# Optimization experiments

Hardware: AMD Instinct MI355X
Metric: run time of the kernel (lower is better)

## Reference

```python
import jax, jax.numpy as jnp
import numpy as np

BLOCK_SIZE = 64
HIDDEN = 1024
INTERMEDIATE = 4096
NUM_BLOCK = HIDDEN // BLOCK_SIZE              # 16
INT_BLOCK = (INTERMEDIATE // HIDDEN) * BLOCK_SIZE  # 256


def setup_inputs() -> dict:
    key = jax.random.key(0)
    k_x, k_w1, k_b1, k_w2, k_b2 = jax.random.split(key, 5)
    hidden_states = jax.random.normal(k_x, (4, 2048, HIDDEN), dtype=jnp.float32)
    w1 = 0.02 * jax.random.normal(k_w1, (NUM_BLOCK, INT_BLOCK, BLOCK_SIZE), dtype=jnp.float32)
    b1 = 0.001 * jax.random.normal(k_b1, (INTERMEDIATE,), dtype=jnp.float32)
    w2 = 0.02 * jax.random.normal(k_w2, (NUM_BLOCK, BLOCK_SIZE, INT_BLOCK), dtype=jnp.float32)
    b2 = 0.001 * jax.random.normal(k_b2, (HIDDEN,), dtype=jnp.float32)
    return {"hidden_states": hidden_states, "w1": w1, "b1": b1, "w2": w2, "b2": b2}


def reference(hidden_states, w1, b1, w2, b2):
    lead = hidden_states.shape[:-1]
    dim = hidden_states.shape[-1]
    nb, ibs, bs = w1.shape  # num_block, intermediate_block_size, block_size
    x = hidden_states.reshape(-1, nb, bs)                 # [B, n, i]
    h = jnp.einsum('bni,noi->bno', x, w1)                 # [B, n, o]
    # channel shuffle: transpose block and feature axes before flattening
    h = jnp.swapaxes(h, -1, -2).reshape(-1, nb * ibs)     # [B, o*n order]
    h = jax.nn.gelu(h + b1, approximate=False)
    h = h.reshape(-1, nb, ibs)                            # regroup after shuffle
    y = jnp.einsum('bni,noi->bno', h, w2).reshape(-1, nb * bs) + b2
    return y.reshape(*lead, dim)
```

## Files before the change

kernel.cpp:

```cpp
#include <hip/hip_runtime.h>
#include <hip/hip_bf16.h>


typedef __attribute__((ext_vector_type(8))) short  short8;
typedef __attribute__((ext_vector_type(4))) short  short4v;
typedef __attribute__((ext_vector_type(4))) float  floatx4;

#define XP 1032

__device__ __forceinline__ short f2bf(float f) {
  union { __hip_bfloat16 h; short s; } u;
  u.h = __float2bfloat16(f);
  return u.s;
}
__device__ __forceinline__ float bf2f(short s) {
  union { float f; unsigned u; } uu;
  uu.u = ((unsigned)(unsigned short)s) << 16;
  return uu.f;
}
__device__ __forceinline__ int pk16(float a, float b) {
  return (int)(unsigned short)f2bf(a) | ((int)(unsigned short)f2bf(b) << 16);
}

__device__ __forceinline__ float gelu_f(float v) {
  float m = v * v;
  float c = fmaf(-0.1029375f, m, -2.3020807f);
  float z = v * c;
  float e = __builtin_amdgcn_exp2f(z);
  return v * __builtin_amdgcn_rcpf(1.0f + e);
}

__global__ void pack_k(const float* __restrict__ w1, const float* __restrict__ w2,
                       const float* __restrict__ b1, short* __restrict__ w1p,
                       short* __restrict__ w2p, short* __restrict__ b1p) {
  const int t = blockIdx.x * blockDim.x + threadIdx.x;
  const int lane = t & 63;
  const int lhi = lane >> 4;
  if (t < 32768) {
    const int ks = (t >> 6) & 1, np = (t >> 7) & 15, n = (t >> 11) & 15;
    const float* src = w1 + ((size_t)(n * 256 + np * 16 + (lane & 15)) * 64 + ks * 32 + lhi * 8);
    short8 f;
#pragma unroll
    for (int e = 0; e < 8; ++e) f[e] = f2bf(src[e]);
    *(short8*)(w1p + (size_t)t * 8) = f;
  } else if (t < 65536) {
    const int t2 = t - 32768;
    const int ot = (t2 >> 6) & 3, s = (t2 >> 8) & 7, np = (t2 >> 11) & 15;
    const int op = ot * 16 + (lane & 15);
    short8 f;
#pragma unroll
    for (int e = 0; e < 8; ++e) {
      const int Kc = 32 * s + 16 * ((e >> 2) & 1) + 4 * lhi + (e & 3);
      const int n = Kc >> 4, ohi = Kc & 15;
      f[e] = f2bf(w2[(size_t)(np * 64 + op) * 256 + ohi * 16 + n]);
    }
    *(short8*)(w2p + (size_t)t2 * 8) = f;
  } else {
    const int t3 = t - 65536;
    const int np = (t3 >> 6) & 15, n = (t3 >> 10) & 15;
    short4v b;
#pragma unroll
    for (int r = 0; r < 4; ++r) b[r] = f2bf(b1[(np * 16 + lhi * 4 + r) * 16 + n]);
    *(short4v*)(b1p + (size_t)((n * 16 + np) * 64 + lane) * 4) = b;
  }
}

__global__ __launch_bounds__(256, 4) void fused_k(
    const float* __restrict__ x, const short* __restrict__ w1p,
    const short* __restrict__ w2p, const short* __restrict__ b1p,
    const float* __restrict__ b2, float* __restrict__ y) {
  __shared__ __align__(16) short xs[16 * XP];

  const int tid = threadIdx.x;
  const int wv = tid >> 6, lane = tid & 63;
  const int l15 = lane & 15, lhi = lane >> 4;
  const int rt  = blockIdx.x >> 2;
  const int np  = (blockIdx.x & 3) * 4 + wv;

#pragma unroll
  for (int p = 0; p < 4; ++p) {
    const int row = wv * 4 + p;
#pragma unroll
    for (int q = 0; q < 4; ++q) {
      const int col = q * 256 + lane * 4;
      floatx4 v = *(const floatx4*)(x + (size_t)(rt * 16 + row) * 1024 + col);
      short4v sv;
#pragma unroll
      for (int e = 0; e < 4; ++e) sv[e] = f2bf(v[e]);
      *(short4v*)(&xs[row * XP + col]) = sv;
    }
  }
  __syncthreads();

  floatx4 c0 = {0.f,0.f,0.f,0.f}, c1 = {0.f,0.f,0.f,0.f};
  floatx4 c2 = {0.f,0.f,0.f,0.f}, c3 = {0.f,0.f,0.f,0.f};

#pragma unroll
  for (int s = 0; s < 8; ++s) {
    int pka0, pka1, pkb0, pkb1;

    {
      const int n = 2 * s;
      short8 xf0 = *(const short8*)(&xs[l15 * XP + n * 64 + lhi * 8]);
      short8 xf1 = *(const short8*)(&xs[l15 * XP + n * 64 + 32 + lhi * 8]);
      short8 wf0 = *(const short8*)(w1p + (size_t)(((n * 16 + np) * 2 + 0) * 64 + lane) * 8);
      short8 wf1 = *(const short8*)(w1p + (size_t)(((n * 16 + np) * 2 + 1) * 64 + lane) * 8);
      short4v bv = *(const short4v*)(b1p + (size_t)((n * 16 + np) * 64 + lane) * 4);
      floatx4 acc = {0.f, 0.f, 0.f, 0.f};
      acc = __builtin_amdgcn_mfma_f32_16x16x32_bf16(wf0, xf0, acc, 0, 0, 0);
      acc = __builtin_amdgcn_mfma_f32_16x16x32_bf16(wf1, xf1, acc, 0, 0, 0);
      const float g0 = gelu_f(acc[0] + bf2f(bv[0]));
      const float g1 = gelu_f(acc[1] + bf2f(bv[1]));
      const float g2 = gelu_f(acc[2] + bf2f(bv[2]));
      const float g3 = gelu_f(acc[3] + bf2f(bv[3]));
      pka0 = pk16(g0, g1);
      pka1 = pk16(g2, g3);
    }
    {
      const int n = 2 * s + 1;
      short8 xf0 = *(const short8*)(&xs[l15 * XP + n * 64 + lhi * 8]);
      short8 xf1 = *(const short8*)(&xs[l15 * XP + n * 64 + 32 + lhi * 8]);
      short8 wf0 = *(const short8*)(w1p + (size_t)(((n * 16 + np) * 2 + 0) * 64 + lane) * 8);
      short8 wf1 = *(const short8*)(w1p + (size_t)(((n * 16 + np) * 2 + 1) * 64 + lane) * 8);
      short4v bv = *(const short4v*)(b1p + (size_t)((n * 16 + np) * 64 + lane) * 4);
      floatx4 acc = {0.f, 0.f, 0.f, 0.f};
      acc = __builtin_amdgcn_mfma_f32_16x16x32_bf16(wf0, xf0, acc, 0, 0, 0);
      acc = __builtin_amdgcn_mfma_f32_16x16x32_bf16(wf1, xf1, acc, 0, 0, 0);
      const float g0 = gelu_f(acc[0] + bf2f(bv[0]));
      const float g1 = gelu_f(acc[1] + bf2f(bv[1]));
      const float g2 = gelu_f(acc[2] + bf2f(bv[2]));
      const float g3 = gelu_f(acc[3] + bf2f(bv[3]));
      pkb0 = pk16(g0, g1);
      pkb1 = pk16(g2, g3);
    }

    union { int i[4]; short8 v; } af;
    af.i[0] = pka0; af.i[1] = pka1; af.i[2] = pkb0; af.i[3] = pkb1;
    const size_t wb = (size_t)((np * 8 + s) * 4) * 64 * 8;
    short8 bf0 = *(const short8*)(w2p + wb + (size_t)(0 * 64 + lane) * 8);
    short8 bf1 = *(const short8*)(w2p + wb + (size_t)(1 * 64 + lane) * 8);
    short8 bf2v = *(const short8*)(w2p + wb + (size_t)(2 * 64 + lane) * 8);
    short8 bf3 = *(const short8*)(w2p + wb + (size_t)(3 * 64 + lane) * 8);
    c0 = __builtin_amdgcn_mfma_f32_16x16x32_bf16(af.v, bf0, c0, 0, 0, 0);
    c1 = __builtin_amdgcn_mfma_f32_16x16x32_bf16(af.v, bf1, c1, 0, 0, 0);
    c2 = __builtin_amdgcn_mfma_f32_16x16x32_bf16(af.v, bf2v, c2, 0, 0, 0);
    c3 = __builtin_amdgcn_mfma_f32_16x16x32_bf16(af.v, bf3, c3, 0, 0, 0);
  }

  floatx4 cc[4] = {c0, c1, c2, c3};
#pragma unroll
  for (int ot = 0; ot < 4; ++ot) {
    const int col = np * 64 + ot * 16 + l15;
    const float bb = b2[col];
    float* py = y + (size_t)(rt * 16 + lhi * 4) * 1024 + col;
#pragma unroll
    for (int r = 0; r < 4; ++r)
      py[(size_t)r * 1024] = cc[ot][r] + bb;
  }
}

extern "C" void kernel_launch(void* const* d_in, const int* in_sizes, int n_in,
                              void* d_out, int out_size, void* d_ws, size_t ws_size,
                              hipStream_t stream) {
  const float* x  = (const float*)d_in[0];
  const float* w1 = (const float*)d_in[1];
  const float* b1 = (const float*)d_in[2];
  const float* w2 = (const float*)d_in[3];
  const float* b2 = (const float*)d_in[4];
  float* y = (float*)d_out;

  short* w1p = (short*)d_ws;
  short* w2p = w1p + 16 * 256 * 64;
  short* b1p = w2p + 16 * 256 * 64;

  pack_k<<<160, 512, 0, stream>>>(w1, w2, b1, w1p, w2p, b1p);
  fused_k<<<2048, 256, 0, stream>>>(x, w1p, w2p, b1p, b2, y);
}
```

Baseline: 47.49 us.

## Software-pipeline weight loads with double-buffered registers and remap block order

Replaces the unrolled loop with an explicit two-stage register double buffer: the loads for step s+1 are issued before the compute of step s, with sched_barriers pinning that order. Occupancy drops from 4 to 3 blocks per SIMD to leave room for the extra registers. Block indexing now walks row tiles fastest instead of output slices. Loads of x and stores of y use nontemporal hints. The intent is to hide global weight-load latency behind the MFMA and GELU work, at the cost of higher register pressure, fewer resident waves and different L2 reuse of x across blocks.

```diff
diff --git a/kernel.cpp b/kernel.cpp
--- a/kernel.cpp
+++ b/kernel.cpp
@@ -65,7 +65,49 @@
   }
 }
 
-__global__ __launch_bounds__(256, 4) void fused_k(
+#define DECLF(F) \
+  short8 F##wf00, F##wf01, F##wf10, F##wf11, F##bf0, F##bf1, F##bf2, F##bf3, \
+         F##xa0, F##xa1, F##xb0, F##xb1; \
+  short4v F##bv0, F##bv1;
+
+#define LOADS(F, s) { \
+  const int n0_ = 2 * (s), n1_ = 2 * (s) + 1; \
+  F##wf00 = *(const short8*)(w1p + (size_t)(((n0_ * 16 + np) * 2 + 0) * 64 + lane) * 8); \
+  F##wf01 = *(const short8*)(w1p + (size_t)(((n0_ * 16 + np) * 2 + 1) * 64 + lane) * 8); \
+  F##wf10 = *(const short8*)(w1p + (size_t)(((n1_ * 16 + np) * 2 + 0) * 64 + lane) * 8); \
+  F##wf11 = *(const short8*)(w1p + (size_t)(((n1_ * 16 + np) * 2 + 1) * 64 + lane) * 8); \
+  F##bv0  = *(const short4v*)(b1p + (size_t)((n0_ * 16 + np) * 64 + lane) * 4); \
+  F##bv1  = *(const short4v*)(b1p + (size_t)((n1_ * 16 + np) * 64 + lane) * 4); \
+  F##bf0  = *(const short8*)(w2p + (size_t)(((np * 8 + (s)) * 4 + 0) * 64 + lane) * 8); \
+  F##bf1  = *(const short8*)(w2p + (size_t)(((np * 8 + (s)) * 4 + 1) * 64 + lane) * 8); \
+  F##bf2  = *(const short8*)(w2p + (size_t)(((np * 8 + (s)) * 4 + 2) * 64 + lane) * 8); \
+  F##bf3  = *(const short8*)(w2p + (size_t)(((np * 8 + (s)) * 4 + 3) * 64 + lane) * 8); \
+  F##xa0  = *(const short8*)(&xs[l15 * XP + n0_ * 64 + lhi * 8]); \
+  F##xa1  = *(const short8*)(&xs[l15 * XP + n0_ * 64 + 32 + lhi * 8]); \
+  F##xb0  = *(const short8*)(&xs[l15 * XP + n1_ * 64 + lhi * 8]); \
+  F##xb1  = *(const short8*)(&xs[l15 * XP + n1_ * 64 + 32 + lhi * 8]); \
+}
+
+#define STEPC(F) { \
+  floatx4 a0_ = {0.f,0.f,0.f,0.f}, a1_ = {0.f,0.f,0.f,0.f}; \
+  a0_ = __builtin_amdgcn_mfma_f32_16x16x32_bf16(F##wf00, F##xa0, a0_, 0, 0, 0); \
+  a0_ = __builtin_amdgcn_mfma_f32_16x16x32_bf16(F##wf01, F##xa1, a0_, 0, 0, 0); \
+  a1_ = __builtin_amdgcn_mfma_f32_16x16x32_bf16(F##wf10, F##xb0, a1_, 0, 0, 0); \
+  a1_ = __builtin_amdgcn_mfma_f32_16x16x32_bf16(F##wf11, F##xb1, a1_, 0, 0, 0); \
+  union { int i[4]; short8 v; } af_; \
+  af_.i[0] = pk16(gelu_f(a0_[0] + bf2f(F##bv0[0])), gelu_f(a0_[1] + bf2f(F##bv0[1]))); \
+  af_.i[1] = pk16(gelu_f(a0_[2] + bf2f(F##bv0[2])), gelu_f(a0_[3] + bf2f(F##bv0[3]))); \
+  af_.i[2] = pk16(gelu_f(a1_[0] + bf2f(F##bv1[0])), gelu_f(a1_[1] + bf2f(F##bv1[1]))); \
+  af_.i[3] = pk16(gelu_f(a1_[2] + bf2f(F##bv1[2])), gelu_f(a1_[3] + bf2f(F##bv1[3]))); \
+  c0 = __builtin_amdgcn_mfma_f32_16x16x32_bf16(af_.v, F##bf0, c0, 0, 0, 0); \
+  c1 = __builtin_amdgcn_mfma_f32_16x16x32_bf16(af_.v, F##bf1, c1, 0, 0, 0); \
+  c2 = __builtin_amdgcn_mfma_f32_16x16x32_bf16(af_.v, F##bf2, c2, 0, 0, 0); \
+  c3 = __builtin_amdgcn_mfma_f32_16x16x32_bf16(af_.v, F##bf3, c3, 0, 0, 0); \
+}
+
+#define SB __builtin_amdgcn_sched_barrier(0);
+
+__global__ __launch_bounds__(256, 3) void fused_k(
     const float* __restrict__ x, const short* __restrict__ w1p,
     const short* __restrict__ w2p, const short* __restrict__ b1p,
     const float* __restrict__ b2, float* __restrict__ y) {
@@ -74,8 +116,8 @@
   const int tid = threadIdx.x;
   const int wv = tid >> 6, lane = tid & 63;
   const int l15 = lane & 15, lhi = lane >> 4;
-  const int rt  = blockIdx.x >> 2;
-  const int np  = (blockIdx.x & 3) * 4 + wv;
+  const int rt  = blockIdx.x & 511;
+  const int np  = (blockIdx.x >> 9) * 4 + wv;
 
 #pragma unroll
   for (int p = 0; p < 4; ++p) {
@@ -83,7 +125,8 @@
 #pragma unroll
     for (int q = 0; q < 4; ++q) {
       const int col = q * 256 + lane * 4;
-      floatx4 v = *(const floatx4*)(x + (size_t)(rt * 16 + row) * 1024 + col);
+      floatx4 v = __builtin_nontemporal_load(
+          (const floatx4*)(x + (size_t)(rt * 16 + row) * 1024 + col));
       short4v sv;
 #pragma unroll
       for (int e = 0; e < 4; ++e) sv[e] = f2bf(v[e]);
@@ -95,57 +138,17 @@
   floatx4 c0 = {0.f,0.f,0.f,0.f}, c1 = {0.f,0.f,0.f,0.f};
   floatx4 c2 = {0.f,0.f,0.f,0.f}, c3 = {0.f,0.f,0.f,0.f};
 
-#pragma unroll
-  for (int s = 0; s < 8; ++s) {
-    int pka0, pka1, pkb0, pkb1;
+  DECLF(A) DECLF(B)
 
-    {
-      const int n = 2 * s;
-      short8 xf0 = *(const short8*)(&xs[l15 * XP + n * 64 + lhi * 8]);
-      short8 xf1 = *(const short8*)(&xs[l15 * XP + n * 64 + 32 + lhi * 8]);
-      short8 wf0 = *(const short8*)(w1p + (size_t)(((n * 16 + np) * 2 + 0) * 64 + lane) * 8);
-      short8 wf1 = *(const short8*)(w1p + (size_t)(((n * 16 + np) * 2 + 1) * 64 + lane) * 8);
-      short4v bv = *(const short4v*)(b1p + (size_t)((n * 16 + np) * 64 + lane) * 4);
-      floatx4 acc = {0.f, 0.f, 0.f, 0.f};
-      acc = __builtin_amdgcn_mfma_f32_16x16x32_bf16(wf0, xf0, acc, 0, 0, 0);
-      acc = __builtin_amdgcn_mfma_f32_16x16x32_bf16(wf1, xf1, acc, 0, 0, 0);
-      const float g0 = gelu_f(acc[0] + bf2f(bv[0]));
-      const float g1 = gelu_f(acc[1] + bf2f(bv[1]));
-      const float g2 = gelu_f(acc[2] + bf2f(bv[2]));
-      const float g3 = gelu_f(acc[3] + bf2f(bv[3]));
-      pka0 = pk16(g0, g1);
-      pka1 = pk16(g2, g3);
-    }
-    {
-      const int n = 2 * s + 1;
-      short8 xf0 = *(const short8*)(&xs[l15 * XP + n * 64 + lhi * 8]);
-      short8 xf1 = *(const short8*)(&xs[l15 * XP + n * 64 + 32 + lhi * 8]);
-      short8 wf0 = *(const short8*)(w1p + (size_t)(((n * 16 + np) * 2 + 0) * 64 + lane) * 8);
-      short8 wf1 = *(const short8*)(w1p + (size_t)(((n * 16 + np) * 2 + 1) * 64 + lane) * 8);
-      short4v bv = *(const short4v*)(b1p + (size_t)((n * 16 + np) * 64 + lane) * 4);
-      floatx4 acc = {0.f, 0.f, 0.f, 0.f};
-      acc = __builtin_amdgcn_mfma_f32_16x16x32_bf16(wf0, xf0, acc, 0, 0, 0);
-      acc = __builtin_amdgcn_mfma_f32_16x16x32_bf16(wf1, xf1, acc, 0, 0, 0);
-      const float g0 = gelu_f(acc[0] + bf2f(bv[0]));
-      const float g1 = gelu_f(acc[1] + bf2f(bv[1]));
-      const float g2 = gelu_f(acc[2] + bf2f(bv[2]));
-      const float g3 = gelu_f(acc[3] + bf2f(bv[3]));
-      pkb0 = pk16(g0, g1);
-      pkb1 = pk16(g2, g3);
-    }
-
-    union { int i[4]; short8 v; } af;
-    af.i[0] = pka0; af.i[1] = pka1; af.i[2] = pkb0; af.i[3] = pkb1;
-    const size_t wb = (size_t)((np * 8 + s) * 4) * 64 * 8;
-    short8 bf0 = *(const short8*)(w2p + wb + (size_t)(0 * 64 + lane) * 8);
-    short8 bf1 = *(const short8*)(w2p + wb + (size_t)(1 * 64 + lane) * 8);
-    short8 bf2v = *(const short8*)(w2p + wb + (size_t)(2 * 64 + lane) * 8);
-    short8 bf3 = *(const short8*)(w2p + wb + (size_t)(3 * 64 + lane) * 8);
-    c0 = __builtin_amdgcn_mfma_f32_16x16x32_bf16(af.v, bf0, c0, 0, 0, 0);
-    c1 = __builtin_amdgcn_mfma_f32_16x16x32_bf16(af.v, bf1, c1, 0, 0, 0);
-    c2 = __builtin_amdgcn_mfma_f32_16x16x32_bf16(af.v, bf2v, c2, 0, 0, 0);
-    c3 = __builtin_amdgcn_mfma_f32_16x16x32_bf16(af.v, bf3, c3, 0, 0, 0);
-  }
+  LOADS(A, 0)
+  LOADS(B, 1) SB STEPC(A)
+  LOADS(A, 2) SB STEPC(B)
+  LOADS(B, 3) SB STEPC(A)
+  LOADS(A, 4) SB STEPC(B)
+  LOADS(B, 5) SB STEPC(A)
+  LOADS(A, 6) SB STEPC(B)
+  LOADS(B, 7) SB STEPC(A)
+  SB STEPC(B)
 
   floatx4 cc[4] = {c0, c1, c2, c3};
 #pragma unroll
@@ -155,7 +158,7 @@
     float* py = y + (size_t)(rt * 16 + lhi * 4) * 1024 + col;
 #pragma unroll
     for (int r = 0; r < 4; ++r)
-      py[(size_t)r * 1024] = cc[ot][r] + bb;
+      __builtin_nontemporal_store(cc[ot][r] + bb, py + (size_t)r * 1024);
   }
 }
 
```

Measured after the change: 56.42 us. +18.8%, slower.

## Replace LDS staging of x with direct global loads and lane permutes

Applied to the files above, without the earlier changes.

Removes the shared-memory tile of bf16 activations and its barrier. Each wave now loads its own x fragments directly from global memory with nontemporal loads, converts them to bf16, and redistributes them across lanes with ds_bpermute to form the MFMA operand layout. The block index mapping also changes so row tiles vary fastest. This aims to lift the LDS occupancy limit and remove the sync, at the cost of less coalesced global reads and weaker L2 locality for the column groups that share the same rows.

```diff
diff --git a/kernel.cpp b/kernel.cpp
--- a/kernel.cpp
+++ b/kernel.cpp
@@ -5,8 +5,6 @@
 typedef __attribute__((ext_vector_type(8))) short  short8;
 typedef __attribute__((ext_vector_type(4))) short  short4v;
 typedef __attribute__((ext_vector_type(4))) float  floatx4;
-
-#define XP 1032
 
 __device__ __forceinline__ short f2bf(float f) {
   union { __hip_bfloat16 h; short s; } u;
@@ -69,82 +67,65 @@
     const float* __restrict__ x, const short* __restrict__ w1p,
     const short* __restrict__ w2p, const short* __restrict__ b1p,
     const float* __restrict__ b2, float* __restrict__ y) {
-  __shared__ __align__(16) short xs[16 * XP];
-
   const int tid = threadIdx.x;
   const int wv = tid >> 6, lane = tid & 63;
   const int l15 = lane & 15, lhi = lane >> 4;
-  const int rt  = blockIdx.x >> 2;
-  const int np  = (blockIdx.x & 3) * 4 + wv;
+  const int rt  = blockIdx.x & 511;
+  const int np  = (blockIdx.x >> 9) * 4 + wv;
 
-#pragma unroll
-  for (int p = 0; p < 4; ++p) {
-    const int row = wv * 4 + p;
-#pragma unroll
-    for (int q = 0; q < 4; ++q) {
-      const int col = q * 256 + lane * 4;
-      floatx4 v = *(const floatx4*)(x + (size_t)(rt * 16 + row) * 1024 + col);
-      short4v sv;
-#pragma unroll
-      for (int e = 0; e < 4; ++e) sv[e] = f2bf(v[e]);
-      *(short4v*)(&xs[row * XP + col]) = sv;
-    }
-  }
-  __syncthreads();
+  const float* xbase = x + (size_t)(rt * 16 + (lane >> 2)) * 1024 + (lane & 3) * 8;
+  const int pidx = (((l15 << 2) | lhi) << 2);
 
   floatx4 c0 = {0.f,0.f,0.f,0.f}, c1 = {0.f,0.f,0.f,0.f};
   floatx4 c2 = {0.f,0.f,0.f,0.f}, c3 = {0.f,0.f,0.f,0.f};
 
 #pragma unroll
   for (int s = 0; s < 8; ++s) {
-    int pka0, pka1, pkb0, pkb1;
+    union { int i[4]; short8 v; } af;
 
-    {
-      const int n = 2 * s;
-      short8 xf0 = *(const short8*)(&xs[l15 * XP + n * 64 + lhi * 8]);
-      short8 xf1 = *(const short8*)(&xs[l15 * XP + n * 64 + 32 + lhi * 8]);
+#pragma unroll
+    for (int half = 0; half < 2; ++half) {
+      const int n = 2 * s + half;
+      const float* p0 = xbase + n * 64;
+      const float* p1 = p0 + 32;
+      floatx4 q0 = __builtin_nontemporal_load((const floatx4*)p0);
+      floatx4 q1 = __builtin_nontemporal_load((const floatx4*)(p0 + 4));
+      floatx4 q2 = __builtin_nontemporal_load((const floatx4*)p1);
+      floatx4 q3 = __builtin_nontemporal_load((const floatx4*)(p1 + 4));
       short8 wf0 = *(const short8*)(w1p + (size_t)(((n * 16 + np) * 2 + 0) * 64 + lane) * 8);
       short8 wf1 = *(const short8*)(w1p + (size_t)(((n * 16 + np) * 2 + 1) * 64 + lane) * 8);
       short4v bv = *(const short4v*)(b1p + (size_t)((n * 16 + np) * 64 + lane) * 4);
+
+      const int i00 = pk16(q0[0], q0[1]), i01 = pk16(q0[2], q0[3]);
+      const int i02 = pk16(q1[0], q1[1]), i03 = pk16(q1[2], q1[3]);
+      const int i10 = pk16(q2[0], q2[1]), i11 = pk16(q2[2], q2[3]);
+      const int i12 = pk16(q3[0], q3[1]), i13 = pk16(q3[2], q3[3]);
+      union { int i[4]; short8 v; } xf0, xf1;
+      xf0.i[0] = __builtin_amdgcn_ds_bpermute(pidx, i00);
+      xf0.i[1] = __builtin_amdgcn_ds_bpermute(pidx, i01);
+      xf0.i[2] = __builtin_amdgcn_ds_bpermute(pidx, i02);
+      xf0.i[3] = __builtin_amdgcn_ds_bpermute(pidx, i03);
+      xf1.i[0] = __builtin_amdgcn_ds_bpermute(pidx, i10);
+      xf1.i[1] = __builtin_amdgcn_ds_bpermute(pidx, i11);
+      xf1.i[2] = __builtin_amdgcn_ds_bpermute(pidx, i12);
+      xf1.i[3] = __builtin_amdgcn_ds_bpermute(pidx, i13);
+
       floatx4 acc = {0.f, 0.f, 0.f, 0.f};
-      acc = __builtin_amdgcn_mfma_f32_16x16x32_bf16(wf0, xf0, acc, 0, 0, 0);
-      acc = __builtin_amdgcn_mfma_f32_16x16x32_bf16(wf1, xf1, acc, 0, 0, 0);
-      const float g0 = gelu_f(acc[0] + bf2f(bv[0]));
-      const float g1 = gelu_f(acc[1] + bf2f(bv[1]));
-      const float g2 = gelu_f(acc[2] + bf2f(bv[2]));
-      const float g3 = gelu_f(acc[3] + bf2f(bv[3]));
-      pka0 = pk16(g0, g1);
-      pka1 = pk16(g2, g3);
-    }
-    {
-      const int n = 2 * s + 1;
-      short8 xf0 = *(const short8*)(&xs[l15 * XP + n * 64 + lhi * 8]);
-      short8 xf1 = *(const short8*)(&xs[l15 * XP + n * 64 + 32 + lhi * 8]);
-      short8 wf0 = *(const short8*)(w1p + (size_t)(((n * 16 + np) * 2 + 0) * 64 + lane) * 8);
-      short8 wf1 = *(const short8*)(w1p + (size_t)(((n * 16 + np) * 2 + 1) * 64 + lane) * 8);
-      short4v bv = *(const short4v*)(b1p + (size_t)((n * 16 + np) * 64 + lane) * 4);
-      floatx4 acc = {0.f, 0.f, 0.f, 0.f};
-      acc = __builtin_amdgcn_mfma_f32_16x16x32_bf16(wf0, xf0, acc, 0, 0, 0);
-      acc = __builtin_amdgcn_mfma_f32_16x16x32_bf16(wf1, xf1, acc, 0, 0, 0);
-      const float g0 = gelu_f(acc[0] + bf2f(bv[0]));
-      const float g1 = gelu_f(acc[1] + bf2f(bv[1]));
-      const float g2 = gelu_f(acc[2] + bf2f(bv[2]));
-      const float g3 = gelu_f(acc[3] + bf2f(bv[3]));
-      pkb0 = pk16(g0, g1);
-      pkb1 = pk16(g2, g3);
+      acc = __builtin_amdgcn_mfma_f32_16x16x32_bf16(wf0, xf0.v, acc, 0, 0, 0);
+      acc = __builtin_amdgcn_mfma_f32_16x16x32_bf16(wf1, xf1.v, acc, 0, 0, 0);
+      af.i[2 * half + 0] = pk16(gelu_f(acc[0] + bf2f(bv[0])), gelu_f(acc[1] + bf2f(bv[1])));
+      af.i[2 * half + 1] = pk16(gelu_f(acc[2] + bf2f(bv[2])), gelu_f(acc[3] + bf2f(bv[3])));
     }
 
-    union { int i[4]; short8 v; } af;
-    af.i[0] = pka0; af.i[1] = pka1; af.i[2] = pkb0; af.i[3] = pkb1;
     const size_t wb = (size_t)((np * 8 + s) * 4) * 64 * 8;
-    short8 bf0 = *(const short8*)(w2p + wb + (size_t)(0 * 64 + lane) * 8);
-    short8 bf1 = *(const short8*)(w2p + wb + (size_t)(1 * 64 + lane) * 8);
+    short8 bf0  = *(const short8*)(w2p + wb + (size_t)(0 * 64 + lane) * 8);
+    short8 bf1  = *(const short8*)(w2p + wb + (size_t)(1 * 64 + lane) * 8);
     short8 bf2v = *(const short8*)(w2p + wb + (size_t)(2 * 64 + lane) * 8);
-    short8 bf3 = *(const short8*)(w2p + wb + (size_t)(3 * 64 + lane) * 8);
-    c0 = __builtin_amdgcn_mfma_f32_16x16x32_bf16(af.v, bf0, c0, 0, 0, 0);
-    c1 = __builtin_amdgcn_mfma_f32_16x16x32_bf16(af.v, bf1, c1, 0, 0, 0);
+    short8 bf3  = *(const short8*)(w2p + wb + (size_t)(3 * 64 + lane) * 8);
+    c0 = __builtin_amdgcn_mfma_f32_16x16x32_bf16(af.v, bf0,  c0, 0, 0, 0);
+    c1 = __builtin_amdgcn_mfma_f32_16x16x32_bf16(af.v, bf1,  c1, 0, 0, 0);
     c2 = __builtin_amdgcn_mfma_f32_16x16x32_bf16(af.v, bf2v, c2, 0, 0, 0);
-    c3 = __builtin_amdgcn_mfma_f32_16x16x32_bf16(af.v, bf3, c3, 0, 0, 0);
+    c3 = __builtin_amdgcn_mfma_f32_16x16x32_bf16(af.v, bf3,  c3, 0, 0, 0);
   }
 
   floatx4 cc[4] = {c0, c1, c2, c3};
```

Result: slower. 113.8 us (+139.6%).
